# Kernel tuning notes

Measured on AMD Instinct MI355X. Metric: run time of the kernel, lower is better.

The kernel has to match this reference:

```python
import jax, jax.numpy as jnp
import numpy as np

B, D, E, H, L, T = 512, 64, 512, 1024, 2, 96
LN_EPS = 1e-5


def setup_inputs() -> dict:
    key = jax.random.key(0)
    ks = jax.random.split(key, 20)
    r = lambda k, shape, sc=0.05: (jax.random.normal(k, shape, jnp.float32) * sc)
    inp = {
        "x_0": jax.random.normal(ks[0], (B, D), jnp.float32),
        "h_n": jax.random.normal(ks[1], (L, B, H), jnp.float32) * 0.1,
        "c_n": jax.random.normal(ks[2], (L, B, H), jnp.float32) * 0.1,
        "forecast_window": T,
        # share_embedding: Linear(D -> E)
        "emb_W": r(ks[3], (D, E)),
        "emb_b": r(ks[4], (E,)),
        # LSTM layer 0: input E -> hidden H ; gates order (i, f, g, o)
        "W_ih0": r(ks[5], (E, 4 * H)),
        "W_hh0": r(ks[6], (H, 4 * H)),
        "b_ih0": r(ks[7], (4 * H,)),
        "b_hh0": r(ks[8], (4 * H,)),
        # LSTM layer 1: input H -> hidden H
        "W_ih1": r(ks[9], (H, 4 * H)),
        "W_hh1": r(ks[10], (H, 4 * H)),
        "b_ih1": r(ks[11], (4 * H,)),
        "b_hh1": r(ks[12], (4 * H,)),
        # fc: Linear(H,H) -> LayerNorm(H) -> ReLU -> Linear(H,D)
        "fc1_W": r(ks[13], (H, H)),
        "fc1_b": r(ks[14], (H,)),
        "ln_g": jnp.ones((H,), jnp.float32),
        "ln_b": jnp.zeros((H,), jnp.float32),
        "fc2_W": r(ks[15], (H, D)),
        "fc2_b": r(ks[16], (D,)),
    }
    return inp


def _lstm_cell(x, h, c, Wih, Whh, b):
    gates = x @ Wih + h @ Whh + b  # [B, 4H]
    i, f, g, o = jnp.split(gates, 4, axis=-1)
    c2 = jax.nn.sigmoid(f) * c + jax.nn.sigmoid(i) * jnp.tanh(g)
    h2 = jax.nn.sigmoid(o) * jnp.tanh(c2)
    return h2, c2


def reference(x_0, h_n, c_n, forecast_window, emb_W, emb_b,
              W_ih0, W_hh0, b_ih0, b_hh0, W_ih1, W_hh1, b_ih1, b_hh1,
              fc1_W, fc1_b, ln_g, ln_b, fc2_W, fc2_b):
    b0 = b_ih0 + b_hh0
    b1 = b_ih1 + b_hh1

    def step(carry, _):
        x, h0, c0, h1, c1 = carry
        xe = x @ emb_W + emb_b                      # embedding
        h0, c0 = _lstm_cell(xe, h0, c0, W_ih0, W_hh0, b0)
        h1, c1 = _lstm_cell(h0, h1, c1, W_ih1, W_hh1, b1)
        z = h1 @ fc1_W + fc1_b                      # Linear
        mu = jnp.mean(z, axis=-1, keepdims=True)    # LayerNorm
        var = jnp.mean((z - mu) ** 2, axis=-1, keepdims=True)
        z = (z - mu) * jax.lax.rsqrt(var + LN_EPS) * ln_g + ln_b
        y = jax.nn.relu(z) @ fc2_W + fc2_b          # ReLU -> Linear
        return (y, h0, c0, h1, c1), y

    carry0 = (x_0, h_n[0], c_n[0], h_n[1], c_n[1])
    _, ys = jax.lax.scan(step, carry0, None, length=int(forecast_window))
    return jnp.transpose(ys, (1, 0, 2))  # [B, T, D]
```

## Files before the change

kernel.cpp:

```cpp
#include <hip/hip_runtime.h>
#include <hip/hip_bf16.h>

using bf16 = __hip_bfloat16;
using short8 = __attribute__((ext_vector_type(8))) short;
using f32x4 = __attribute__((ext_vector_type(4))) float;

#define BB 512
#define HH 1024
#define DD 64
#define TT 96

__device__ __forceinline__ void load_lds16(const void* g, void* l) {
  __builtin_amdgcn_global_load_lds(
      (const __attribute__((address_space(1))) unsigned int*)g,
      (__attribute__((address_space(3))) unsigned int*)l, 16, 0, 0);
}

__device__ __forceinline__ float sigm(float x) { return 1.0f / (1.0f + __expf(-x)); }
__device__ __forceinline__ float tanh_f(float x) {
  float e = __expf(2.0f * x);
  return 1.0f - 2.0f / (e + 1.0f);
}
__device__ __forceinline__ float wred(float v) {
#pragma unroll
  for (int m = 1; m < 64; m <<= 1) v += __shfl_xor(v, m, 64);
  return v;
}


__global__ __launch_bounds__(256) void init_states_k(
    const float* __restrict__ x0, const float* __restrict__ hn, const float* __restrict__ cn,
    bf16* __restrict__ xbh, bf16* __restrict__ xbl,
    bf16* __restrict__ h0h, bf16* __restrict__ h0l,
    bf16* __restrict__ h1h, bf16* __restrict__ h1l,
    float* __restrict__ c0, float* __restrict__ c1)
{
  int i = blockIdx.x * 256 + threadIdx.x;
  if (i < BB * HH) {
    float v0 = hn[i];
    bf16 a0 = __float2bfloat16(v0);
    h0h[i] = a0; h0l[i] = __float2bfloat16(v0 - __bfloat162float(a0));
    float v1 = hn[BB * HH + i];
    bf16 a1 = __float2bfloat16(v1);
    h1h[i] = a1; h1l[i] = __float2bfloat16(v1 - __bfloat162float(a1));
    c0[i] = cn[i];
    c1[i] = cn[BB * HH + i];
  }
  if (i < BB * DD) {
    float v = x0[i];
    bf16 a = __float2bfloat16(v);
    xbh[i] = a; xbl[i] = __float2bfloat16(v - __bfloat162float(a));
  }
}

__device__ __forceinline__ int gate_perm(int c) {
  int g = c >> 10, n = c & 1023;
  return (n >> 5) * 128 + g * 32 + (n & 31);
}

__global__ __launch_bounds__(256) void fold_emb_k(
    const float* __restrict__ embW, const float* __restrict__ embB,
    const float* __restrict__ Wih0, const float* __restrict__ bih0, const float* __restrict__ bhh0,
    bf16* __restrict__ W0h, bf16* __restrict__ W0l, float* __restrict__ bias0)
{
  __shared__ float sW[512 * 8];
  __shared__ float sb[512];
  int tid = threadIdx.x;
  int d0 = blockIdx.y * 8;
  for (int i = tid; i < 4096; i += 256) {
    int j = i >> 9;
    int e = i & 511;
    sW[e * 8 + j] = embW[(size_t)(d0 + j) * 512 + e];
  }
  for (int i = tid; i < 512; i += 256) sb[i] = embB[i];
  __syncthreads();
  int c = blockIdx.x * 256 + tid;
  float acc[8] = {0, 0, 0, 0, 0, 0, 0, 0};
  float bacc = 0.0f;
  for (int e = 0; e < 512; ++e) {
    float wv = Wih0[(size_t)e * 4096 + c];
    float4 wa = *(const float4*)&sW[e * 8];
    float4 wb = *(const float4*)&sW[e * 8 + 4];
    acc[0] += wa.x * wv; acc[1] += wa.y * wv; acc[2] += wa.z * wv; acc[3] += wa.w * wv;
    acc[4] += wb.x * wv; acc[5] += wb.y * wv; acc[6] += wb.z * wv; acc[7] += wb.w * wv;
    bacc += sb[e] * wv;
  }
  int pr = gate_perm(c);
#pragma unroll
  for (int j = 0; j < 8; ++j) {
    float v = acc[j];
    bf16 h = __float2bfloat16(v);
    W0h[(size_t)pr * 1088 + d0 + j] = h;
    W0l[(size_t)pr * 1088 + d0 + j] = __float2bfloat16(v - __bfloat162float(h));
  }
  if (blockIdx.y == 0) bias0[pr] = bacc + bih0[c] + bhh0[c];
}

template <bool PERM>
__global__ __launch_bounds__(256) void transpose_conv_k(
    const float* __restrict__ src, int N,
    bf16* __restrict__ dsth, bf16* __restrict__ dstl, int dstStride, int k0)
{
  __shared__ float tb[32][33];
  int tx = threadIdx.x & 31;
  int ty = threadIdx.x >> 5;
  int c0 = blockIdx.x * 32;
  int kk0 = blockIdx.y * 32;
#pragma unroll
  for (int q = 0; q < 4; ++q) {
    int k = kk0 + q * 8 + ty;
    tb[q * 8 + ty][tx] = src[(size_t)k * N + c0 + tx];
  }
  __syncthreads();
#pragma unroll
  for (int q = 0; q < 4; ++q) {
    int cc = c0 + q * 8 + ty;
    int pr = PERM ? gate_perm(cc) : cc;
    float v = tb[tx][q * 8 + ty];
    bf16 h = __float2bfloat16(v);
    size_t di = (size_t)pr * dstStride + k0 + kk0 + tx;
    dsth[di] = h;
    dstl[di] = __float2bfloat16(v - __bfloat162float(h));
  }
}

__global__ __launch_bounds__(256) void bias_perm_k(
    const float* __restrict__ a, const float* __restrict__ b, float* __restrict__ out)
{
  int c = blockIdx.x * 256 + threadIdx.x;
  out[gate_perm(c)] = a[c] + b[c];
}

template <int EPI>
__global__ __launch_bounds__(128) void gemm_step_k(
    const bf16* __restrict__ A1h, const bf16* __restrict__ A1l, int lda1, int K1len,
    const bf16* __restrict__ A2h, const bf16* __restrict__ A2l, int lda2,
    const bf16* __restrict__ Bth, const bf16* __restrict__ Btl, int KTOT,
    const float* __restrict__ bias,
    float* __restrict__ zout,
    float* __restrict__ cstate,
    bf16* __restrict__ houth, bf16* __restrict__ houtl,
    int nPanels)
{
  __shared__ __align__(16) char smem[40960];
  const int tid = threadIdx.x;
  const int lane = tid & 63;
  const int wv = tid >> 6;
  const int bid = blockIdx.x;
  const int npanel = bid % nPanels;
  const int m0 = (bid / nPanels) * 32;
  const int nrow0 = npanel * 128;

  f32x4 acc[8] = {};
  const int ntiles = KTOT >> 5;

  auto stage = [&](int qbuf, int kt) {
    char* lb = smem + qbuf * 20480;
    {
      int row = tid >> 2, sl = tid & 3;
      int sb = (sl * 16) ^ (((row >> 2) & 3) << 4);
      int ke = kt + (sb >> 1);
      const bf16 *gh, *gl;
      if (kt < K1len) {
        gh = A1h + (size_t)(m0 + row) * lda1 + ke;
        gl = A1l + (size_t)(m0 + row) * lda1 + ke;
      } else {
        gh = A2h + (size_t)(m0 + row) * lda2 + (ke - K1len);
        gl = A2l + (size_t)(m0 + row) * lda2 + (ke - K1len);
      }
      load_lds16((const void*)gh, (void*)(lb + tid * 16));
      load_lds16((const void*)gl, (void*)(lb + 2048 + tid * 16));
    }
#pragma unroll
    for (int q = 0; q < 4; ++q) {
      int L = q * 128 + tid;
      int row = L >> 2, sl = L & 3;
      int sb = (sl * 16) ^ (((row >> 2) & 3) << 4);
      int ke = kt + (sb >> 1);
      load_lds16((const void*)(Bth + (size_t)(nrow0 + row) * KTOT + ke),
                 (void*)(lb + 4096 + L * 16));
      load_lds16((const void*)(Btl + (size_t)(nrow0 + row) * KTOT + ke),
                 (void*)(lb + 12288 + L * 16));
    }
  };

  stage(0, 0);
  __syncthreads();
  const int l15 = lane & 15;
  const int lhi = lane >> 4;
  const int kb = lhi * 16;
  const int arow = wv * 16 + l15;
  const int aoff = arow * 64 + (kb ^ (((arow >> 2) & 3) << 4));

  for (int t = 0; t < ntiles; ++t) {
    int cur = t & 1;
    if (t + 1 < ntiles) stage(cur ^ 1, (t + 1) << 5);
    const char* base = smem + cur * 20480;
    short8 ah = *(const short8*)(base + aoff);
    short8 al = *(const short8*)(base + 2048 + aoff);
#pragma unroll
    for (int f = 0; f < 8; ++f) {
      int brow = f * 16 + l15;
      int boff = brow * 64 + (kb ^ (((brow >> 2) & 3) << 4));
      short8 bh = *(const short8*)(base + 4096 + boff);
      short8 bl = *(const short8*)(base + 12288 + boff);
      acc[f] = __builtin_amdgcn_mfma_f32_16x16x32_bf16(ah, bh, acc[f], 0, 0, 0);
      acc[f] = __builtin_amdgcn_mfma_f32_16x16x32_bf16(ah, bl, acc[f], 0, 0, 0);
      acc[f] = __builtin_amdgcn_mfma_f32_16x16x32_bf16(al, bh, acc[f], 0, 0, 0);
    }
    __syncthreads();
  }

  if (EPI == 0) {
#pragma unroll
    for (int s = 0; s < 2; ++s) {
      f32x4 ai = acc[0 + s], af = acc[2 + s], ag = acc[4 + s], ao = acc[6 + s];
      int unit = npanel * 32 + s * 16 + l15;
      int prb = npanel * 128 + s * 16 + l15;
      float bi = bias[prb + 0];
      float bfv = bias[prb + 32];
      float bg = bias[prb + 64];
      float bo = bias[prb + 96];
#pragma unroll
      for (int r = 0; r < 4; ++r) {
        int row = m0 + wv * 16 + lhi * 4 + r;
        float iv = ai[r] + bi;
        float fv = af[r] + bfv;
        float gv = ag[r] + bg;
        float ov = ao[r] + bo;
        size_t idx = (size_t)row * HH + unit;
        float co = cstate[idx];
        float cn2 = sigm(fv) * co + sigm(iv) * tanh_f(gv);
        cstate[idx] = cn2;
        float hv = sigm(ov) * tanh_f(cn2);
        bf16 hh = __float2bfloat16(hv);
        houth[idx] = hh;
        houtl[idx] = __float2bfloat16(hv - __bfloat162float(hh));
      }
    }
  } else {
#pragma unroll
    for (int f = 0; f < 8; ++f) {
      int col = npanel * 128 + f * 16 + l15;
      float bb = bias[col];
#pragma unroll
      for (int r = 0; r < 4; ++r) {
        int row = m0 + wv * 16 + lhi * 4 + r;
        zout[(size_t)row * HH + col] = acc[f][r] + bb;
      }
    }
  }
}

__global__ __launch_bounds__(256) void ln_fc2_k(
    const float* __restrict__ z, const float* __restrict__ lng, const float* __restrict__ lnb,
    const float* __restrict__ W2 , const float* __restrict__ b2,
    float* __restrict__ out ,
    bf16* __restrict__ xbh, bf16* __restrict__ xbl, int tstep)
{
  __shared__ float sa[4][1024];
  __shared__ float red[4][4][64];
  int tid = threadIdx.x, lane = tid & 63, w = tid >> 6;
  int row = blockIdx.x * 4 + w;
  float zv[16];
#pragma unroll
  for (int j = 0; j < 16; ++j) zv[j] = z[(size_t)row * 1024 + j * 64 + lane];
  float s = 0;
#pragma unroll
  for (int j = 0; j < 16; ++j) s += zv[j];
  s = wred(s);
  float mu = s * (1.0f / 1024.0f);
  float vs = 0;
#pragma unroll
  for (int j = 0; j < 16; ++j) { float d = zv[j] - mu; vs += d * d; }
  vs = wred(vs);
  float rstd = rsqrtf(vs * (1.0f / 1024.0f) + 1e-5f);
#pragma unroll
  for (int j = 0; j < 16; ++j) {
    int k = j * 64 + lane;
    float a = (zv[j] - mu) * rstd * lng[k] + lnb[k];
    sa[w][k] = a > 0.0f ? a : 0.0f;
  }
  __syncthreads();
  int n = tid & 63, ks = (tid >> 6) * 256;
  float p0 = 0, p1 = 0, p2 = 0, p3 = 0;
  for (int k = ks; k < ks + 256; ++k) {
    float wv2 = W2[(size_t)k * 64 + n];
    p0 += sa[0][k] * wv2; p1 += sa[1][k] * wv2; p2 += sa[2][k] * wv2; p3 += sa[3][k] * wv2;
  }
  int sl = tid >> 6;
  red[0][sl][n] = p0; red[1][sl][n] = p1; red[2][sl][n] = p2; red[3][sl][n] = p3;
  __syncthreads();
  int rr = tid >> 6;
  float y = red[rr][0][n] + red[rr][1][n] + red[rr][2][n] + red[rr][3][n] + b2[n];
  int orow = blockIdx.x * 4 + rr;
  out[((size_t)orow * TT + tstep) * DD + n] = y;
  bf16 hh = __float2bfloat16(y);
  xbh[(size_t)orow * DD + n] = hh;
  xbl[(size_t)orow * DD + n] = __float2bfloat16(y - __bfloat162float(hh));
}


extern "C" void kernel_launch(void* const* d_in, const int* in_sizes, int n_in,
                              void* d_out, int out_size, void* d_ws, size_t ws_size,
                              hipStream_t stream)
{
  const float* x0   = (const float*)d_in[0];
  const float* hn   = (const float*)d_in[1];
  const float* cn   = (const float*)d_in[2];
  const float* embW = (const float*)d_in[4];
  const float* embB = (const float*)d_in[5];
  const float* Wih0 = (const float*)d_in[6];
  const float* Whh0 = (const float*)d_in[7];
  const float* bih0 = (const float*)d_in[8];
  const float* bhh0 = (const float*)d_in[9];
  const float* Wih1 = (const float*)d_in[10];
  const float* Whh1 = (const float*)d_in[11];
  const float* bih1 = (const float*)d_in[12];
  const float* bhh1 = (const float*)d_in[13];
  const float* fc1W = (const float*)d_in[14];
  const float* fc1b = (const float*)d_in[15];
  const float* lng  = (const float*)d_in[16];
  const float* lnb  = (const float*)d_in[17];
  const float* fc2W = (const float*)d_in[18];
  const float* fc2b = (const float*)d_in[19];

  char* wp = (char*)d_ws;
  size_t off = 0;
  auto alloc = [&](size_t bytes) -> void* {
    void* p = wp + off;
    off += (bytes + 255) & ~(size_t)255;
    return p;
  };

  bf16* W0th  = (bf16*)alloc((size_t)4096 * 1088 * 2);
  bf16* W0tl  = (bf16*)alloc((size_t)4096 * 1088 * 2);
  bf16* W1th  = (bf16*)alloc((size_t)4096 * 2048 * 2);
  bf16* W1tl  = (bf16*)alloc((size_t)4096 * 2048 * 2);
  bf16* f1h   = (bf16*)alloc((size_t)1024 * 1024 * 2);
  bf16* f1l   = (bf16*)alloc((size_t)1024 * 1024 * 2);
  float* bias0 = (float*)alloc(4096 * 4);
  float* bias1 = (float*)alloc(4096 * 4);
  bf16* xbh   = (bf16*)alloc((size_t)BB * DD * 2);
  bf16* xbl   = (bf16*)alloc((size_t)BB * DD * 2);
  bf16* h0h_a = (bf16*)alloc((size_t)BB * HH * 2);
  bf16* h0h_b = (bf16*)alloc((size_t)BB * HH * 2);
  bf16* h0l_a = (bf16*)alloc((size_t)BB * HH * 2);
  bf16* h0l_b = (bf16*)alloc((size_t)BB * HH * 2);
  bf16* h1h_a = (bf16*)alloc((size_t)BB * HH * 2);
  bf16* h1h_b = (bf16*)alloc((size_t)BB * HH * 2);
  bf16* h1l_a = (bf16*)alloc((size_t)BB * HH * 2);
  bf16* h1l_b = (bf16*)alloc((size_t)BB * HH * 2);
  float* c0   = (float*)alloc((size_t)BB * HH * 4);
  float* c1   = (float*)alloc((size_t)BB * HH * 4);
  float* z    = (float*)alloc((size_t)BB * HH * 4);

  init_states_k<<<2048, 256, 0, stream>>>(x0, hn, cn, xbh, xbl, h0h_a, h0l_a, h1h_a, h1l_a, c0, c1);
  fold_emb_k<<<dim3(16, 8), 256, 0, stream>>>(embW, embB, Wih0, bih0, bhh0, W0th, W0tl, bias0);
  transpose_conv_k<true><<<dim3(128, 32), 256, 0, stream>>>(Whh0, 4096, W0th, W0tl, 1088, 64);
  transpose_conv_k<true><<<dim3(128, 32), 256, 0, stream>>>(Wih1, 4096, W1th, W1tl, 2048, 0);
  transpose_conv_k<true><<<dim3(128, 32), 256, 0, stream>>>(Whh1, 4096, W1th, W1tl, 2048, 1024);
  transpose_conv_k<false><<<dim3(32, 32), 256, 0, stream>>>(fc1W, 1024, f1h, f1l, 1024, 0);
  bias_perm_k<<<16, 256, 0, stream>>>(bih1, bhh1, bias1);

  bf16* h0h[2] = {h0h_a, h0h_b};
  bf16* h0l[2] = {h0l_a, h0l_b};
  bf16* h1h[2] = {h1h_a, h1h_b};
  bf16* h1l[2] = {h1l_a, h1l_b};
  float* outp = (float*)d_out;

  for (int t = 0; t < TT; ++t) {
    int p = t & 1;
    gemm_step_k<0><<<512, 128, 0, stream>>>(
        xbh, xbl, DD, DD, h0h[p], h0l[p], HH, W0th, W0tl, 1088, bias0,
        nullptr, c0, h0h[p ^ 1], h0l[p ^ 1], 32);
    gemm_step_k<0><<<512, 128, 0, stream>>>(
        h0h[p ^ 1], h0l[p ^ 1], HH, HH, h1h[p], h1l[p], HH, W1th, W1tl, 2048, bias1,
        nullptr, c1, h1h[p ^ 1], h1l[p ^ 1], 32);
    gemm_step_k<1><<<128, 128, 0, stream>>>(
        h1h[p ^ 1], h1l[p ^ 1], HH, 1024, h1h[p ^ 1], h1l[p ^ 1], HH, f1h, f1l, 1024,
        fc1b, z, nullptr, nullptr, nullptr, 8);
    ln_fc2_k<<<128, 256, 0, stream>>>(z, lng, lnb, fc2W, fc2b, outp, xbh, xbl, t);
  }
}
```

Before: 10.66 ms.

## Enlarge GEMM tiles to 64x128 with four-stage async LDS pipeline

The per-step GEMM kernel now computes 64x128 output tiles per block instead of 32x128. Each wave holds a 4x4 fragment grid, which raises operand reuse from LDS. It keeps a four-buffer LDS ring with three tiles in flight, using explicit vmcnt waits instead of double buffering with a full __syncthreads each iteration. The gate permutation moves to 16-wide groups so each wave owns whole i/f/g/o columns in the fused LSTM epilogue. This halves the grid size (only 64 blocks for fc1), which risks lower occupancy and CU utilisation, and uses 96KB of LDS per block.

```diff
diff --git a/kernel.cpp b/kernel.cpp
--- a/kernel.cpp
+++ b/kernel.cpp
@@ -25,6 +25,11 @@
 #pragma unroll
   for (int m = 1; m < 64; m <<= 1) v += __shfl_xor(v, m, 64);
   return v;
+}
+
+__device__ __forceinline__ int gate_perm(int c) {
+  int g = c >> 10, n = c & 1023;
+  return (n >> 4) * 64 + g * 16 + (n & 15);
 }
 
 
@@ -51,11 +56,6 @@
     bf16 a = __float2bfloat16(v);
     xbh[i] = a; xbl[i] = __float2bfloat16(v - __bfloat162float(a));
   }
-}
-
-__device__ __forceinline__ int gate_perm(int c) {
-  int g = c >> 10, n = c & 1023;
-  return (n >> 5) * 128 + g * 32 + (n & 31);
 }
 
 __global__ __launch_bounds__(256) void fold_emb_k(
@@ -132,44 +132,44 @@
 }
 
 template <int EPI>
-__global__ __launch_bounds__(128) void gemm_step_k(
+__global__ __launch_bounds__(128) void gemm_pipe_k(
     const bf16* __restrict__ A1h, const bf16* __restrict__ A1l, int lda1, int K1len,
     const bf16* __restrict__ A2h, const bf16* __restrict__ A2l, int lda2,
-    const bf16* __restrict__ Bth, const bf16* __restrict__ Btl, int KTOT,
+    const bf16* __restrict__ Bh, const bf16* __restrict__ Bl, int KTOT,
     const float* __restrict__ bias,
-    float* __restrict__ zout,
-    float* __restrict__ cstate,
-    bf16* __restrict__ houth, bf16* __restrict__ houtl,
+    float* __restrict__ zout, float* __restrict__ cst,
+    bf16* __restrict__ hho, bf16* __restrict__ hlo,
     int nPanels)
 {
-  __shared__ __align__(16) char smem[40960];
-  const int tid = threadIdx.x;
-  const int lane = tid & 63;
-  const int wv = tid >> 6;
+  __shared__ __align__(16) char smem[98304];
+  const int tid = threadIdx.x, lane = tid & 63, wv = tid >> 6;
   const int bid = blockIdx.x;
   const int npanel = bid % nPanels;
-  const int m0 = (bid / nPanels) * 32;
+  const int m0 = (bid / nPanels) * 64;
   const int nrow0 = npanel * 128;
-
-  f32x4 acc[8] = {};
-  const int ntiles = KTOT >> 5;
-
-  auto stage = [&](int qbuf, int kt) {
-    char* lb = smem + qbuf * 20480;
-    {
-      int row = tid >> 2, sl = tid & 3;
+  const int l15 = lane & 15, lhi = lane >> 4, kb = lhi * 16;
+
+  f32x4 acc[16];
+#pragma unroll
+  for (int i = 0; i < 16; ++i) acc[i] = f32x4{0, 0, 0, 0};
+
+  const int nt = KTOT >> 5;
+
+  auto stage = [&](int buf, int kt) {
+    char* lb = smem + buf * 24576;
+    bool first = kt < K1len;
+#pragma unroll
+    for (int q = 0; q < 2; ++q) {
+      int L = q * 128 + tid;
+      int row = L >> 2, sl = L & 3;
       int sb = (sl * 16) ^ (((row >> 2) & 3) << 4);
       int ke = kt + (sb >> 1);
-      const bf16 *gh, *gl;
-      if (kt < K1len) {
-        gh = A1h + (size_t)(m0 + row) * lda1 + ke;
-        gl = A1l + (size_t)(m0 + row) * lda1 + ke;
-      } else {
-        gh = A2h + (size_t)(m0 + row) * lda2 + (ke - K1len);
-        gl = A2l + (size_t)(m0 + row) * lda2 + (ke - K1len);
-      }
-      load_lds16((const void*)gh, (void*)(lb + tid * 16));
-      load_lds16((const void*)gl, (void*)(lb + 2048 + tid * 16));
+      const bf16* gh = first ? A1h + (size_t)(m0 + row) * lda1 + ke
+                             : A2h + (size_t)(m0 + row) * lda2 + (ke - K1len);
+      const bf16* gl = first ? A1l + (size_t)(m0 + row) * lda1 + ke
+                             : A2l + (size_t)(m0 + row) * lda2 + (ke - K1len);
+      load_lds16(gh, lb + L * 16);
+      load_lds16(gl, lb + 4096 + L * 16);
     }
 #pragma unroll
     for (int q = 0; q < 4; ++q) {
@@ -177,78 +177,90 @@
       int row = L >> 2, sl = L & 3;
       int sb = (sl * 16) ^ (((row >> 2) & 3) << 4);
       int ke = kt + (sb >> 1);
-      load_lds16((const void*)(Bth + (size_t)(nrow0 + row) * KTOT + ke),
-                 (void*)(lb + 4096 + L * 16));
-      load_lds16((const void*)(Btl + (size_t)(nrow0 + row) * KTOT + ke),
-                 (void*)(lb + 12288 + L * 16));
+      load_lds16(Bh + (size_t)(nrow0 + row) * KTOT + ke, lb + 8192 + L * 16);
+      load_lds16(Bl + (size_t)(nrow0 + row) * KTOT + ke, lb + 16384 + L * 16);
     }
   };
 
   stage(0, 0);
-  __syncthreads();
-  const int l15 = lane & 15;
-  const int lhi = lane >> 4;
-  const int kb = lhi * 16;
-  const int arow = wv * 16 + l15;
-  const int aoff = arow * 64 + (kb ^ (((arow >> 2) & 3) << 4));
-
-  for (int t = 0; t < ntiles; ++t) {
-    int cur = t & 1;
-    if (t + 1 < ntiles) stage(cur ^ 1, (t + 1) << 5);
-    const char* base = smem + cur * 20480;
-    short8 ah = *(const short8*)(base + aoff);
-    short8 al = *(const short8*)(base + 2048 + aoff);
-#pragma unroll
-    for (int f = 0; f < 8; ++f) {
-      int brow = f * 16 + l15;
+  if (nt > 1) stage(1, 32);
+  if (nt > 2) stage(2, 64);
+
+  for (int t = 0; t < nt; ++t) {
+    int ahead = nt - 1 - t;
+    if (ahead >= 2)      asm volatile("s_waitcnt vmcnt(24)" ::: "memory");
+    else if (ahead == 1) asm volatile("s_waitcnt vmcnt(12)" ::: "memory");
+    else                 asm volatile("s_waitcnt vmcnt(0)"  ::: "memory");
+    asm volatile("s_waitcnt lgkmcnt(0)" ::: "memory");
+    __builtin_amdgcn_s_barrier();
+    __builtin_amdgcn_sched_barrier(0);
+    if (t + 3 < nt) stage((t + 3) & 3, (t + 3) << 5);
+    const char* base = smem + (t & 3) * 24576;
+    short8 ah[4], al[4], bh[4], bl[4];
+#pragma unroll
+    for (int mf = 0; mf < 4; ++mf) {
+      int arow = mf * 16 + l15;
+      int aoff = arow * 64 + (kb ^ (((arow >> 2) & 3) << 4));
+      ah[mf] = *(const short8*)(base + aoff);
+      al[mf] = *(const short8*)(base + 4096 + aoff);
+    }
+#pragma unroll
+    for (int nf = 0; nf < 4; ++nf) {
+      int brow = wv * 64 + nf * 16 + l15;
       int boff = brow * 64 + (kb ^ (((brow >> 2) & 3) << 4));
-      short8 bh = *(const short8*)(base + 4096 + boff);
-      short8 bl = *(const short8*)(base + 12288 + boff);
-      acc[f] = __builtin_amdgcn_mfma_f32_16x16x32_bf16(ah, bh, acc[f], 0, 0, 0);
-      acc[f] = __builtin_amdgcn_mfma_f32_16x16x32_bf16(ah, bl, acc[f], 0, 0, 0);
-      acc[f] = __builtin_amdgcn_mfma_f32_16x16x32_bf16(al, bh, acc[f], 0, 0, 0);
-    }
-    __syncthreads();
+      bh[nf] = *(const short8*)(base + 8192 + boff);
+      bl[nf] = *(const short8*)(base + 16384 + boff);
+    }
+#pragma unroll
+    for (int mf = 0; mf < 4; ++mf)
+#pragma unroll
+      for (int nf = 0; nf < 4; ++nf) {
+        f32x4 c = acc[mf * 4 + nf];
+        c = __builtin_amdgcn_mfma_f32_16x16x32_bf16(ah[mf], bh[nf], c, 0, 0, 0);
+        c = __builtin_amdgcn_mfma_f32_16x16x32_bf16(ah[mf], bl[nf], c, 0, 0, 0);
+        c = __builtin_amdgcn_mfma_f32_16x16x32_bf16(al[mf], bh[nf], c, 0, 0, 0);
+        acc[mf * 4 + nf] = c;
+      }
   }
 
   if (EPI == 0) {
-#pragma unroll
-    for (int s = 0; s < 2; ++s) {
-      f32x4 ai = acc[0 + s], af = acc[2 + s], ag = acc[4 + s], ao = acc[6 + s];
-      int unit = npanel * 32 + s * 16 + l15;
-      int prb = npanel * 128 + s * 16 + l15;
-      float bi = bias[prb + 0];
-      float bfv = bias[prb + 32];
-      float bg = bias[prb + 64];
-      float bo = bias[prb + 96];
+    const int unit = npanel * 32 + wv * 16 + l15;
+    const int prb = npanel * 128 + wv * 64 + l15;
+    float bi = bias[prb + 0];
+    float bfv = bias[prb + 16];
+    float bg = bias[prb + 32];
+    float bo = bias[prb + 48];
+#pragma unroll
+    for (int mf = 0; mf < 4; ++mf) {
+      f32x4 ai = acc[mf * 4 + 0], af = acc[mf * 4 + 1];
+      f32x4 ag = acc[mf * 4 + 2], ao = acc[mf * 4 + 3];
 #pragma unroll
       for (int r = 0; r < 4; ++r) {
-        int row = m0 + wv * 16 + lhi * 4 + r;
-        float iv = ai[r] + bi;
-        float fv = af[r] + bfv;
-        float gv = ag[r] + bg;
-        float ov = ao[r] + bo;
+        int row = m0 + mf * 16 + lhi * 4 + r;
         size_t idx = (size_t)row * HH + unit;
-        float co = cstate[idx];
+        float iv = ai[r] + bi, fv = af[r] + bfv, gv = ag[r] + bg, ov = ao[r] + bo;
+        float co = cst[idx];
         float cn2 = sigm(fv) * co + sigm(iv) * tanh_f(gv);
-        cstate[idx] = cn2;
+        cst[idx] = cn2;
         float hv = sigm(ov) * tanh_f(cn2);
         bf16 hh = __float2bfloat16(hv);
-        houth[idx] = hh;
-        houtl[idx] = __float2bfloat16(hv - __bfloat162float(hh));
+        hho[idx] = hh;
+        hlo[idx] = __float2bfloat16(hv - __bfloat162float(hh));
       }
     }
   } else {
 #pragma unroll
-    for (int f = 0; f < 8; ++f) {
-      int col = npanel * 128 + f * 16 + l15;
-      float bb = bias[col];
-#pragma unroll
-      for (int r = 0; r < 4; ++r) {
-        int row = m0 + wv * 16 + lhi * 4 + r;
-        zout[(size_t)row * HH + col] = acc[f][r] + bb;
+    for (int mf = 0; mf < 4; ++mf)
+#pragma unroll
+      for (int nf = 0; nf < 4; ++nf) {
+        int col = npanel * 128 + wv * 64 + nf * 16 + l15;
+        float bb = bias[col];
+#pragma unroll
+        for (int r = 0; r < 4; ++r) {
+          int row = m0 + mf * 16 + lhi * 4 + r;
+          zout[(size_t)row * HH + col] = acc[mf * 4 + nf][r] + bb;
+        }
       }
-    }
   }
 }
 
@@ -355,7 +367,8 @@
   float* c1   = (float*)alloc((size_t)BB * HH * 4);
   float* z    = (float*)alloc((size_t)BB * HH * 4);
 
-  init_states_k<<<2048, 256, 0, stream>>>(x0, hn, cn, xbh, xbl, h0h_a, h0l_a, h1h_a, h1l_a, c0, c1);
+  init_states_k<<<2048, 256, 0, stream>>>(x0, hn, cn, xbh, xbl, h0h_a, h0l_a,
+                                          h1h_a, h1l_a, c0, c1);
   fold_emb_k<<<dim3(16, 8), 256, 0, stream>>>(embW, embB, Wih0, bih0, bhh0, W0th, W0tl, bias0);
   transpose_conv_k<true><<<dim3(128, 32), 256, 0, stream>>>(Whh0, 4096, W0th, W0tl, 1088, 64);
   transpose_conv_k<true><<<dim3(128, 32), 256, 0, stream>>>(Wih1, 4096, W1th, W1tl, 2048, 0);
@@ -371,13 +384,13 @@
 
   for (int t = 0; t < TT; ++t) {
     int p = t & 1;
-    gemm_step_k<0><<<512, 128, 0, stream>>>(
+    gemm_pipe_k<0><<<256, 128, 0, stream>>>(
         xbh, xbl, DD, DD, h0h[p], h0l[p], HH, W0th, W0tl, 1088, bias0,
         nullptr, c0, h0h[p ^ 1], h0l[p ^ 1], 32);
-    gemm_step_k<0><<<512, 128, 0, stream>>>(
+    gemm_pipe_k<0><<<256, 128, 0, stream>>>(
         h0h[p ^ 1], h0l[p ^ 1], HH, HH, h1h[p], h1l[p], HH, W1th, W1tl, 2048, bias1,
         nullptr, c1, h1h[p ^ 1], h1l[p ^ 1], 32);
-    gemm_step_k<1><<<128, 128, 0, stream>>>(
+    gemm_pipe_k<1><<<64, 128, 0, stream>>>(
         h1h[p ^ 1], h1l[p ^ 1], HH, 1024, h1h[p ^ 1], h1l[p ^ 1], HH, f1h, f1l, 1024,
         fc1b, z, nullptr, nullptr, nullptr, 8);
     ln_fc2_k<<<128, 256, 0, stream>>>(z, lng, lnb, fc2W, fc2b, outp, xbh, xbl, t);
```

After: 11.52 ms. +8.0%, slower.
